# Kernel optimization log

Measured on AMD Instinct MI355X. Metric: run time of the kernel, lower is better.

Reference implementation:

```python
import jax, jax.numpy as jnp
import numpy as np

N, S, D, H, E, ETYPES = 1024, 64, 256, 4, 4096, 4
HD = D // H
EPS = 1e-5


def setup_inputs() -> dict:
    key = jax.random.key(0)
    ks = jax.random.split(key, 8)
    node_features = jax.random.normal(ks[0], (N, S, D), dtype=jnp.float32)
    lengths = jax.random.randint(ks[1], (N,), 1, S + 1)
    node_masks = (jnp.arange(S)[None, :] < lengths[:, None]).astype(jnp.float32)
    # unique edges (torch builds an adjacency matrix, so duplicates collapse)
    rng = np.random.default_rng(0)
    cand = rng.integers(0, N, size=(4 * E, 2))
    uniq = np.unique(cand, axis=0)
    assert uniq.shape[0] >= E
    perm = rng.permutation(uniq.shape[0])[:E]
    edge_index = jnp.asarray(uniq[perm].T, dtype=jnp.int64)  # [2, E]
    edge_type = jnp.asarray(rng.integers(1, ETYPES + 1, size=(E,)), dtype=jnp.int64)
    scale = 0.02
    wq = jax.random.normal(ks[2], (D, D), jnp.float32) * scale
    wk = jax.random.normal(ks[3], (D, D), jnp.float32) * scale
    wv = jax.random.normal(ks[4], (D, D), jnp.float32) * scale
    wo = jax.random.normal(ks[5], (D, D), jnp.float32) * scale
    return dict(
        node_features=node_features, node_masks=node_masks,
        ln_w=jnp.ones((D,), jnp.float32), ln_b=jnp.zeros((D,), jnp.float32),
        wq=wq, bq=jnp.zeros((D,), jnp.float32),
        wk=wk, bk=jnp.zeros((D,), jnp.float32),
        wv=wv, bv=jnp.zeros((D,), jnp.float32),
        wo=wo, bo=jnp.zeros((D,), jnp.float32),
        edge_type_weights=jnp.ones((ETYPES,), jnp.float32),
        edge_index=edge_index, edge_type=edge_type,
    )


def reference(node_features, node_masks, ln_w, ln_b, wq, bq, wk, bk, wv, bv,
              wo, bo, edge_type_weights, edge_index, edge_type):
    n, s, d = node_features.shape
    # LayerNorm (biased variance, eps=1e-5, as torch)
    mu = jnp.mean(node_features, axis=-1, keepdims=True)
    var = jnp.mean((node_features - mu) ** 2, axis=-1, keepdims=True)
    xn = (node_features - mu) * jax.lax.rsqrt(var + EPS) * ln_w + ln_b
    q = (xn @ wq + bq).reshape(n, s, H, HD)
    k = (xn @ wk + bk).reshape(n, s, H, HD)
    v = (xn @ wv + bv).reshape(n, s, H, HD)
    src, dst = edge_index[0], edge_index[1]
    # per-edge scalar bias: softplus(edge_type_weights[type-1]).clamp(1e-6, 1e6)
    ew = jnp.clip(jax.nn.softplus(edge_type_weights[edge_type - 1]), 1e-6, 1e6)  # [E]
    qe, ke, ve = q[src], k[dst], v[dst]              # [E,S,H,HD]
    km = node_masks[dst]                              # [E,S] key-side mask
    qm = node_masks[src]                              # [E,S] query-side mask
    scores = jnp.einsum('eqhd,ekhd->ehqk', qe, ke) / jnp.sqrt(jnp.float32(HD))
    scores = scores + ew[:, None, None, None]
    neg = jnp.float32(-1e30)
    scores = jnp.where(km[:, None, None, :] > 0, scores, neg)
    # per-edge softmax over the key node's valid tokens; zero rows where no valid key
    attn = jax.nn.softmax(scores, axis=-1) * km[:, None, None, :]
    ctx = jnp.einsum('ehqk,ekhd->eqhd', attn, ve) * qm[:, :, None, None]  # [E,S,H,HD]
    out = jax.ops.segment_sum(ctx, src, num_segments=n)   # sum over incident edges
    out = out.reshape(n, s, d)
    out = out @ wo + bo                                   # output projection (dropout=eval noop)
    out = out + node_features                             # residual
    return out * node_masks[..., None]
```

## Files before the change

kernel.cpp:

```cpp
#include <hip/hip_runtime.h>

#define DDIM 256
#define NEDGE 4096
#define SLEN 64
#define NNODE 1024
#define ROWS 65536

typedef short s16x8 __attribute__((ext_vector_type(8)));
typedef float f32x4 __attribute__((ext_vector_type(4)));

static __device__ __forceinline__ unsigned short f2bf(float f){
  union { float f; unsigned u; } v; v.f = f;
  unsigned r = v.u + 0x7FFFu + ((v.u >> 16) & 1u);
  return (unsigned short)(r >> 16);
}

static __device__ __forceinline__ void gl2lds16(const unsigned short* g, unsigned short* l){
  __builtin_amdgcn_global_load_lds((const __attribute__((address_space(1))) unsigned int*)g,
                                   (__attribute__((address_space(3))) unsigned int*)l, 16, 0, 0);
}

__global__ __launch_bounds__(256) void setup_kernel(const float* nf, const float* lnw, const float* lnb,
                                                    const float* wq, const float* wk, const float* wv, const float* wo,
                                                    const float* bq, const float* bk, const float* bv,
                                                    const float* masks, const int* eidx,
                                                    unsigned short* xn, unsigned short* Wqkv, unsigned short* Wo_t,
                                                    float* qkvb, int* lenp, int* startp, int* order, int* degp, int* elist){
  __shared__ int deg[NNODE];
  __shared__ int buf[256];
  __shared__ int hist[65];
  __shared__ int cur[NNODE];
  int bid = blockIdx.x, tid = threadIdx.x;
  if (bid < 16384){
    int lane = tid & 63;
    int row = bid*4 + (tid >> 6);
    const float4 x4 = ((const float4*)(nf + (size_t)row*DDIM))[lane];
    float s  = x4.x + x4.y + x4.z + x4.w;
    float sq = x4.x*x4.x + x4.y*x4.y + x4.z*x4.z + x4.w*x4.w;
    for (int off=1; off<64; off<<=1){ s += __shfl_xor(s, off); sq += __shfl_xor(sq, off); }
    float mu  = s  * (1.0f/DDIM);
    float var = sq * (1.0f/DDIM) - mu*mu;
    float rs  = rsqrtf(var + 1e-5f);
    float4 w4 = ((const float4*)lnw)[lane];
    float4 b4 = ((const float4*)lnb)[lane];
    ushort4 o;
    o.x = f2bf((x4.x - mu)*rs*w4.x + b4.x);
    o.y = f2bf((x4.y - mu)*rs*w4.y + b4.y);
    o.z = f2bf((x4.z - mu)*rs*w4.z + b4.z);
    o.w = f2bf((x4.w - mu)*rs*w4.w + b4.w);
    ((ushort4*)(xn + (size_t)row*DDIM))[lane] = o;
  } else if (bid < 17412){
    int idx = (bid - 16384)*256 + tid;
    if (idx < 196608){
      int mat = idx >> 16;
      int rem = idx & 65535;
      int n = rem >> 8, k = rem & 255;
      const float* W = (mat==0)?wq:(mat==1)?wk:wv;
      Wqkv[(size_t)(mat*256 + n)*256 + k] = f2bf(W[k*256 + n]);
    } else if (idx < 262144){
      int rem = idx - 196608;
      int n = rem >> 8, k = rem & 255;
      Wo_t[(size_t)n*256 + k] = f2bf(wo[k*256 + n]);
    } else if (idx < 262912){
      int i = idx - 262144;
      qkvb[i] = (i < 256) ? bq[i] : (i < 512) ? bk[i-256] : bv[i-512];
    }
  } else if (bid < 17668){
    int lane = tid & 63;
    int node = (bid - 17412)*4 + (tid >> 6);
    unsigned long long b = __ballot(masks[node*SLEN + lane] > 0.f);
    if (lane == 0) lenp[node] = __popcll(b);
  } else {
    int t = tid;
    #pragma unroll
    for (int i=0;i<4;i++) deg[i*256 + t] = 0;
    if (t < 65) hist[t] = 0;
    __syncthreads();
    #pragma unroll
    for (int i=0;i<16;i++) atomicAdd(&deg[eidx[i*256 + t]], 1);
    __syncthreads();
    int d[4]; int s = 0;
    #pragma unroll
    for (int j=0;j<4;j++){ d[j] = deg[t*4 + j]; s += d[j]; }
    buf[t] = s;
    __syncthreads();
    for (int off=1; off<256; off<<=1){
      int v = (t >= off) ? buf[t-off] : 0;
      __syncthreads();
      buf[t] += v;
      __syncthreads();
    }
    int run = buf[t] - s;
    #pragma unroll
    for (int j=0;j<4;j++){
      int node = t*4 + j;
      startp[node] = run; degp[node] = d[j]; cur[node] = run;
      run += d[j];
      int dc = d[j] > 64 ? 64 : d[j];
      atomicAdd(&hist[dc], 1);
    }
    __syncthreads();
    if (t == 0){
      int acc = 0;
      for (int i=64;i>=0;i--){ int h = hist[i]; hist[i] = acc; acc += h; }
    }
    __syncthreads();
    #pragma unroll
    for (int j=0;j<4;j++){
      int node = t*4 + j;
      int dc = d[j] > 64 ? 64 : d[j];
      int pos = atomicAdd(&hist[dc], 1);
      order[pos] = node;
    }
    __syncthreads();
    #pragma unroll
    for (int i=0;i<16;i++){
      int e = i*256 + t;
      int sn = eidx[e];
      int p = atomicAdd(&cur[sn], 1);
      elist[p] = eidx[NEDGE + e];
    }
  }
}

__global__ __launch_bounds__(256) void qkv_kernel(const unsigned short* xn, const unsigned short* Wqkv,
                                                  const float* qkvb, const int* lenp,
                                                  unsigned short* qb, unsigned short* kb_, unsigned short* vt){
  __shared__ __align__(16) unsigned short As[2][8192];
  __shared__ __align__(16) unsigned short Bs[2][8192];
  int tid = threadIdx.x;
  int lane = tid & 63, wid = tid >> 6, m = lane & 15, quad = lane >> 4;
  int row0 = blockIdx.x * 128;
  int nodeA = row0 >> 6;
  int vraA = ((lenp[nodeA]   + 15) >> 4) << 4;
  int vraB = ((lenp[nodeA+1] + 15) >> 4) << 4;
  int col0 = blockIdx.y * 128;
  int wr = wid & 1, wc = wid >> 1;
  int rbase = wr * 64;
  int nodeW = nodeA + wr;
  int qtmW = (wr ? vraB : vraA) >> 4;

  f32x4 acc[16];
  #pragma unroll
  for (int i=0;i<16;i++) acc[i] = (f32x4){0.f,0.f,0.f,0.f};

  #pragma unroll
  for (int i=0;i<4;i++){
    int rowg = i*32 + wid*8;
    bool ok = (rowg < 64) ? (rowg < vraA) : (rowg - 64 < vraB);
    if (ok){
      int cid = i*256 + tid, row = cid >> 3, c8 = cid & 7;
      gl2lds16(xn + (size_t)(row0 + row)*DDIM + ((c8 ^ (row&7))<<3), As[0] + cid*8);
    }
  }
  #pragma unroll
  for (int i=0;i<4;i++){
    int cid = i*256 + tid, row = cid >> 3, c8 = cid & 7;
    gl2lds16(Wqkv + (size_t)(col0 + row)*DDIM + ((c8 ^ (row&7))<<3), Bs[0] + cid*8);
  }

  for (int kc = 0; kc < 4; kc++){
    __syncthreads();
    if (kc < 3){
      int kn = kc + 1;
      #pragma unroll
      for (int i=0;i<4;i++){
        int rowg = i*32 + wid*8;
        bool ok = (rowg < 64) ? (rowg < vraA) : (rowg - 64 < vraB);
        if (ok){
          int cid = i*256 + tid, row = cid >> 3, c8 = cid & 7;
          gl2lds16(xn + (size_t)(row0 + row)*DDIM + kn*64 + ((c8 ^ (row&7))<<3), As[kn&1] + cid*8);
        }
      }
      #pragma unroll
      for (int i=0;i<4;i++){
        int cid = i*256 + tid, row = cid >> 3, c8 = cid & 7;
        gl2lds16(Wqkv + (size_t)(col0 + row)*DDIM + kn*64 + ((c8 ^ (row&7))<<3), Bs[kn&1] + cid*8);
      }
    }
    const unsigned short* Asc = As[kc&1];
    const unsigned short* Bsc = Bs[kc&1];
    #pragma unroll
    for (int ks=0; ks<2; ks++){
      int sw = ((ks*4 + quad) ^ (m&7)) << 3;
      s16x8 af[4], bf[4];
      #pragma unroll
      for (int mt=0;mt<4;mt++) if (mt < qtmW) af[mt] = *(const s16x8*)(Asc + (rbase + mt*16 + m)*64 + sw);
      #pragma unroll
      for (int nt=0;nt<4;nt++) bf[nt] = *(const s16x8*)(Bsc + (wc*64 + nt*16 + m)*64 + sw);
      #pragma unroll
      for (int mt=0;mt<4;mt++) if (mt < qtmW)
        #pragma unroll
        for (int nt=0;nt<4;nt++)
          acc[mt*4+nt] = __builtin_amdgcn_mfma_f32_16x16x32_bf16(af[mt], bf[nt], acc[mt*4+nt], 0,0,0);
    }
  }
  #pragma unroll
  for (int nt=0;nt<4;nt++){
    int cg = col0 + wc*64 + nt*16 + m;
    int mat = cg >> 8, col = cg & 255;
    float bb = qkvb[cg];
    if (mat < 2){
      unsigned short* ob = (mat==0)?qb:kb_;
      #pragma unroll
      for (int mt=0;mt<4;mt++) if (mt < qtmW)
        #pragma unroll
        for (int r=0;r<4;r++){
          int row = row0 + rbase + mt*16 + quad*4 + r;
          ob[(size_t)row*DDIM + col] = f2bf(acc[mt*4+nt][r] + bb);
        }
    } else {
      #pragma unroll
      for (int mt=0;mt<4;mt++) if (mt < qtmW){
        int tok0 = mt*16 + quad*4;
        ushort4 p;
        p.x = f2bf(acc[mt*4+nt][0] + bb);
        p.y = f2bf(acc[mt*4+nt][1] + bb);
        p.z = f2bf(acc[mt*4+nt][2] + bb);
        p.w = f2bf(acc[mt*4+nt][3] + bb);
        *(ushort4*)(vt + ((size_t)nodeW*256 + col)*64 + tok0) = p;
      }
    }
  }
}

__global__ __launch_bounds__(256) void attn_kernel(const unsigned short* qb, const unsigned short* kbuf,
                                                   const unsigned short* vtb, const int* lenp,
                                                   const int* startp, const int* degp, const int* elist,
                                                   const int* order, unsigned short* ctxb){
  __shared__ __align__(16) unsigned short Kt[2][4096];
  __shared__ __align__(16) unsigned short Vt[2][4096];
  __shared__ unsigned short P[4096];
  int tid = threadIdx.x;
  int lane = tid & 63, wid = tid >> 6, m = lane & 15, quad = lane >> 4;
  int src = order[blockIdx.x], h = blockIdx.y;
  int ls = lenp[src];
  int qtm = (ls + 15) >> 4;
  int s0 = startp[src], dg = degp[src];
  bool active = wid < qtm;
  unsigned short* Pw = P + wid*1024;

  s16x8 qf0 = {0,0,0,0,0,0,0,0}, qf1 = {0,0,0,0,0,0,0,0};
  if (active){
    const unsigned short* qbase = qb + (size_t)(src*SLEN + wid*16 + m)*DDIM + h*64 + quad*8;
    qf0 = *(const s16x8*)(qbase);
    qf1 = *(const s16x8*)(qbase + 32);
  }
  f32x4 o[4];
  #pragma unroll
  for (int i=0;i<4;i++) o[i] = (f32x4){0.f,0.f,0.f,0.f};

  int dst0 = 0, dst1 = 0, ld0 = 0;
  if (dg > 0){
    dst0 = elist[s0];
    ld0 = lenp[dst0];
    int kch = ((ld0 + 15) >> 4) * 128;
    #pragma unroll
    for (int i=0;i<2;i++){
      int cid = i*256 + tid;
      if (i*256 + wid*64 < kch){
        int row = cid >> 3, c8 = cid & 7;
        gl2lds16(kbuf + (size_t)(dst0*SLEN + row)*DDIM + h*64 + ((c8 ^ (row&7))<<3), Kt[0] + cid*8);
      }
    }
    const unsigned short* vhead = vtb + ((size_t)dst0*256 + h*64)*64;
    #pragma unroll
    for (int i=0;i<2;i++){
      int cid = i*256 + tid, row = cid >> 3, c8 = cid & 7;
      gl2lds16(vhead + row*64 + ((c8 ^ (row&7))<<3), Vt[0] + cid*8);
    }
  }
  if (dg > 1) dst1 = elist[s0 + 1];
  __syncthreads();

  for (int ei=0; ei<dg; ei++){
    int cur = ei & 1, nxt = cur ^ 1;
    int dst2 = (ei+2 < dg) ? elist[s0 + ei + 2] : 0;
    int ld1 = 0;
    if (ei+1 < dg){
      ld1 = lenp[dst1];
      int kch = ((ld1 + 15) >> 4) * 128;
      #pragma unroll
      for (int i=0;i<2;i++){
        int cid = i*256 + tid;
        if (i*256 + wid*64 < kch){
          int row = cid >> 3, c8 = cid & 7;
          gl2lds16(kbuf + (size_t)(dst1*SLEN + row)*DDIM + h*64 + ((c8 ^ (row&7))<<3), Kt[nxt] + cid*8);
        }
      }
      const unsigned short* vhead = vtb + ((size_t)dst1*256 + h*64)*64;
      #pragma unroll
      for (int i=0;i<2;i++){
        int cid = i*256 + tid, row = cid >> 3, c8 = cid & 7;
        gl2lds16(vhead + row*64 + ((c8 ^ (row&7))<<3), Vt[nxt] + cid*8);
      }
    }
    int ktm = (ld0 + 15) >> 4;
    int ks2 = (ktm + 1) >> 1;
    if (active){
      __builtin_amdgcn_s_setprio(1);
      f32x4 acc[4];
      #pragma unroll
      for (int i=0;i<4;i++) acc[i] = (f32x4){0.f,0.f,0.f,0.f};
      #pragma unroll
      for (int kt=0; kt<4; kt++) if (kt < ktm){
        int key = kt*16 + m;
        s16x8 b0 = *(const s16x8*)(Kt[cur] + key*64 + ((quad ^ (m&7))<<3));
        acc[kt] = __builtin_amdgcn_mfma_f32_16x16x32_bf16(qf0, b0, acc[kt], 0,0,0);
        s16x8 b1 = *(const s16x8*)(Kt[cur] + key*64 + (((4 + quad) ^ (m&7))<<3));
        acc[kt] = __builtin_amdgcn_mfma_f32_16x16x32_bf16(qf1, b1, acc[kt], 0,0,0);
      }
      #pragma unroll
      for (int r=0; r<4; r++){
        float x[4];
        #pragma unroll
        for (int kt=0; kt<4; kt++)
          x[kt] = (kt < ktm && kt*16 + m < ld0) ? __expf(acc[kt][r]*0.125f) : 0.f;
        float s = x[0] + x[1] + x[2] + x[3];
        for (int off=1; off<16; off<<=1) s += __shfl_xor(s, off);
        float inv = 1.0f / s;
        int q = quad*4 + r;
        #pragma unroll
        for (int kt=0; kt<4; kt++) if (kt < 2*ks2){
          int key = kt*16 + m;
          Pw[q*64 + (((key>>3)^(q&7))<<3) + (key&7)] = f2bf(x[kt]*inv);
        }
      }
      #pragma unroll
      for (int ks=0; ks<2; ks++) if (ks < ks2){
        s16x8 pa = *(const s16x8*)(Pw + m*64 + ((((ks*4+quad))^(m&7))<<3));
        #pragma unroll
        for (int dt=0; dt<4; dt++){
          int d = dt*16 + m;
          s16x8 vf = *(const s16x8*)(Vt[cur] + d*64 + (((ks*4+quad)^(d&7))<<3));
          o[dt] = __builtin_amdgcn_mfma_f32_16x16x32_bf16(pa, vf, o[dt], 0,0,0);
        }
      }
      __builtin_amdgcn_s_setprio(0);
    }
    dst0 = dst1; ld0 = ld1; dst1 = dst2;
    __syncthreads();
  }
  if (active){
    #pragma unroll
    for (int dt=0; dt<4; dt++){
      int col = h*64 + dt*16 + m;
      #pragma unroll
      for (int r=0; r<4; r++){
        int row = src*SLEN + wid*16 + quad*4 + r;
        ctxb[(size_t)row*DDIM + col] = f2bf(o[dt][r]);
      }
    }
  }
}

__global__ __launch_bounds__(256) void out_kernel(const unsigned short* ctxb, const unsigned short* Wo_t,
                                                  const float* bo, const float* nf, const float* masks,
                                                  const int* lenp, float* out){
  __shared__ __align__(16) unsigned short As[2][8192];
  __shared__ __align__(16) unsigned short Bs[2][8192];
  int tid = threadIdx.x;
  int lane = tid & 63, wid = tid >> 6, m = lane & 15, quad = lane >> 4;
  int row0 = blockIdx.x * 128;
  int nodeA = row0 >> 6;
  int vraA = ((lenp[nodeA]   + 15) >> 4) << 4;
  int vraB = ((lenp[nodeA+1] + 15) >> 4) << 4;
  int col0 = blockIdx.y * 128;
  int wr = wid & 1, wc = wid >> 1;
  int rbase = wr * 64;
  int qtmW = (wr ? vraB : vraA) >> 4;

  f32x4 acc[16];
  #pragma unroll
  for (int i=0;i<16;i++) acc[i] = (f32x4){0.f,0.f,0.f,0.f};

  #pragma unroll
  for (int i=0;i<4;i++){
    int rowg = i*32 + wid*8;
    bool ok = (rowg < 64) ? (rowg < vraA) : (rowg - 64 < vraB);
    if (ok){
      int cid = i*256 + tid, row = cid >> 3, c8 = cid & 7;
      gl2lds16(ctxb + (size_t)(row0 + row)*DDIM + ((c8 ^ (row&7))<<3), As[0] + cid*8);
    }
  }
  #pragma unroll
  for (int i=0;i<4;i++){
    int cid = i*256 + tid, row = cid >> 3, c8 = cid & 7;
    gl2lds16(Wo_t + (size_t)(col0 + row)*DDIM + ((c8 ^ (row&7))<<3), Bs[0] + cid*8);
  }

  for (int kc = 0; kc < 4; kc++){
    __syncthreads();
    if (kc < 3){
      int kn = kc + 1;
      #pragma unroll
      for (int i=0;i<4;i++){
        int rowg = i*32 + wid*8;
        bool ok = (rowg < 64) ? (rowg < vraA) : (rowg - 64 < vraB);
        if (ok){
          int cid = i*256 + tid, row = cid >> 3, c8 = cid & 7;
          gl2lds16(ctxb + (size_t)(row0 + row)*DDIM + kn*64 + ((c8 ^ (row&7))<<3), As[kn&1] + cid*8);
        }
      }
      #pragma unroll
      for (int i=0;i<4;i++){
        int cid = i*256 + tid, row = cid >> 3, c8 = cid & 7;
        gl2lds16(Wo_t + (size_t)(col0 + row)*DDIM + kn*64 + ((c8 ^ (row&7))<<3), Bs[kn&1] + cid*8);
      }
    }
    const unsigned short* Asc = As[kc&1];
    const unsigned short* Bsc = Bs[kc&1];
    #pragma unroll
    for (int ks=0; ks<2; ks++){
      int sw = ((ks*4 + quad) ^ (m&7)) << 3;
      s16x8 af[4], bf[4];
      #pragma unroll
      for (int mt=0;mt<4;mt++) if (mt < qtmW) af[mt] = *(const s16x8*)(Asc + (rbase + mt*16 + m)*64 + sw);
      #pragma unroll
      for (int nt=0;nt<4;nt++) bf[nt] = *(const s16x8*)(Bsc + (wc*64 + nt*16 + m)*64 + sw);
      #pragma unroll
      for (int mt=0;mt<4;mt++) if (mt < qtmW)
        #pragma unroll
        for (int nt=0;nt<4;nt++)
          acc[mt*4+nt] = __builtin_amdgcn_mfma_f32_16x16x32_bf16(af[mt], bf[nt], acc[mt*4+nt], 0,0,0);
    }
  }
  #pragma unroll
  for (int nt=0;nt<4;nt++){
    int col = col0 + wc*64 + nt*16 + m;
    float bb = bo[col];
    #pragma unroll
    for (int mt=0;mt<4;mt++){
      if (mt < qtmW){
        #pragma unroll
        for (int r=0;r<4;r++){
          int row = row0 + rbase + mt*16 + quad*4 + r;
          float v = acc[mt*4+nt][r] + bb + nf[(size_t)row*DDIM + col];
          out[(size_t)row*DDIM + col] = v * masks[row];
        }
      } else {
        #pragma unroll
        for (int r=0;r<4;r++){
          int row = row0 + rbase + mt*16 + quad*4 + r;
          out[(size_t)row*DDIM + col] = 0.f;
        }
      }
    }
  }
}

extern "C" void kernel_launch(void* const* d_in, const int* in_sizes, int n_in,
                              void* d_out, int out_size, void* d_ws, size_t ws_size,
                              hipStream_t stream){
  const float* nf    = (const float*)d_in[0];
  const float* masks = (const float*)d_in[1];
  const float* lnw   = (const float*)d_in[2];
  const float* lnb   = (const float*)d_in[3];
  const float* wq    = (const float*)d_in[4];
  const float* bq    = (const float*)d_in[5];
  const float* wk    = (const float*)d_in[6];
  const float* bk    = (const float*)d_in[7];
  const float* wv    = (const float*)d_in[8];
  const float* bv    = (const float*)d_in[9];
  const float* wo    = (const float*)d_in[10];
  const float* bo    = (const float*)d_in[11];
  const int*   eidx  = (const int*)d_in[13];
  float* out = (float*)d_out;

  char* ws = (char*)d_ws;
  const size_t B = (size_t)ROWS * DDIM * 2;
  unsigned short* xn   = (unsigned short*)(ws);
  unsigned short* qb   = (unsigned short*)(ws + B);
  unsigned short* kb   = (unsigned short*)(ws + 2*B);
  unsigned short* vt   = (unsigned short*)(ws + 3*B);
  unsigned short* ctxb = (unsigned short*)(ws + 4*B);
  char* wp = ws + 5*B;
  unsigned short* Wqkv = (unsigned short*)(wp);
  unsigned short* Wo_t = (unsigned short*)(wp + 393216);
  float* qkvb         = (float*)(wp + 524288);
  char* ip = wp + 528384;
  int* startp = (int*)(ip);
  int* lenp   = (int*)(ip + 4096);
  int* order  = (int*)(ip + 8192);
  int* degp   = (int*)(ip + 12288);
  int* elist  = (int*)(ip + 16384);

  setup_kernel<<<17669, 256, 0, stream>>>(nf, lnw, lnb, wq, wk, wv, wo, bq, bk, bv,
                                          masks, eidx, xn, Wqkv, Wo_t, qkvb,
                                          lenp, startp, order, degp, elist);
  qkv_kernel<<<dim3(ROWS/128, 6), 256, 0, stream>>>(xn, Wqkv, qkvb, lenp, qb, kb, vt);
  attn_kernel<<<dim3(NNODE, 4), 256, 0, stream>>>(qb, kb, vt, lenp, startp, degp, elist, order, ctxb);
  out_kernel<<<dim3(ROWS/128, 2), 256, 0, stream>>>(ctxb, Wo_t, bo, nf, masks, lenp, out);
}
```

Before: 343.9 us.

## Read K/V fragments straight from global memory instead of staged LDS double buffer

The attention kernel drops its cooperative, double-buffered async staging of each neighbour's K and V tiles into shared memory. Each wave now loads its MFMA operands directly from global (L2-resident) memory, and waves with no valid query tile exit early. Without shared K/V buffers the per-edge __syncthreads disappear, LDS use drops, and more blocks can be resident. In exchange, each active wave re-reads the same K/V data separately and there is no explicit prefetch overlapping the next edge's loads with compute.

```diff
diff --git a/kernel.cpp b/kernel.cpp
--- a/kernel.cpp
+++ b/kernel.cpp
@@ -228,128 +228,77 @@
                                                    const unsigned short* vtb, const int* lenp,
                                                    const int* startp, const int* degp, const int* elist,
                                                    const int* order, unsigned short* ctxb){
-  __shared__ __align__(16) unsigned short Kt[2][4096];
-  __shared__ __align__(16) unsigned short Vt[2][4096];
   __shared__ unsigned short P[4096];
   int tid = threadIdx.x;
   int lane = tid & 63, wid = tid >> 6, m = lane & 15, quad = lane >> 4;
   int src = order[blockIdx.x], h = blockIdx.y;
-  int ls = lenp[src];
-  int qtm = (ls + 15) >> 4;
+  int qtm = (lenp[src] + 15) >> 4;
+  if (wid >= qtm) return;
   int s0 = startp[src], dg = degp[src];
-  bool active = wid < qtm;
   unsigned short* Pw = P + wid*1024;
 
-  s16x8 qf0 = {0,0,0,0,0,0,0,0}, qf1 = {0,0,0,0,0,0,0,0};
-  if (active){
-    const unsigned short* qbase = qb + (size_t)(src*SLEN + wid*16 + m)*DDIM + h*64 + quad*8;
-    qf0 = *(const s16x8*)(qbase);
-    qf1 = *(const s16x8*)(qbase + 32);
-  }
+  const unsigned short* qbase = qb + (size_t)(src*SLEN + wid*16 + m)*DDIM + h*64 + quad*8;
+  s16x8 qf0 = *(const s16x8*)(qbase);
+  s16x8 qf1 = *(const s16x8*)(qbase + 32);
   f32x4 o[4];
   #pragma unroll
   for (int i=0;i<4;i++) o[i] = (f32x4){0.f,0.f,0.f,0.f};
 
-  int dst0 = 0, dst1 = 0, ld0 = 0;
-  if (dg > 0){
-    dst0 = elist[s0];
-    ld0 = lenp[dst0];
-    int kch = ((ld0 + 15) >> 4) * 128;
-    #pragma unroll
-    for (int i=0;i<2;i++){
-      int cid = i*256 + tid;
-      if (i*256 + wid*64 < kch){
-        int row = cid >> 3, c8 = cid & 7;
-        gl2lds16(kbuf + (size_t)(dst0*SLEN + row)*DDIM + h*64 + ((c8 ^ (row&7))<<3), Kt[0] + cid*8);
-      }
-    }
-    const unsigned short* vhead = vtb + ((size_t)dst0*256 + h*64)*64;
-    #pragma unroll
-    for (int i=0;i<2;i++){
-      int cid = i*256 + tid, row = cid >> 3, c8 = cid & 7;
-      gl2lds16(vhead + row*64 + ((c8 ^ (row&7))<<3), Vt[0] + cid*8);
-    }
-  }
-  if (dg > 1) dst1 = elist[s0 + 1];
-  __syncthreads();
-
+  int dstc = 0, ldc = 0;
+  if (dg > 0){ dstc = elist[s0]; ldc = lenp[dstc]; }
   for (int ei=0; ei<dg; ei++){
-    int cur = ei & 1, nxt = cur ^ 1;
-    int dst2 = (ei+2 < dg) ? elist[s0 + ei + 2] : 0;
-    int ld1 = 0;
-    if (ei+1 < dg){
-      ld1 = lenp[dst1];
-      int kch = ((ld1 + 15) >> 4) * 128;
-      #pragma unroll
-      for (int i=0;i<2;i++){
-        int cid = i*256 + tid;
-        if (i*256 + wid*64 < kch){
-          int row = cid >> 3, c8 = cid & 7;
-          gl2lds16(kbuf + (size_t)(dst1*SLEN + row)*DDIM + h*64 + ((c8 ^ (row&7))<<3), Kt[nxt] + cid*8);
-        }
-      }
-      const unsigned short* vhead = vtb + ((size_t)dst1*256 + h*64)*64;
-      #pragma unroll
-      for (int i=0;i<2;i++){
-        int cid = i*256 + tid, row = cid >> 3, c8 = cid & 7;
-        gl2lds16(vhead + row*64 + ((c8 ^ (row&7))<<3), Vt[nxt] + cid*8);
-      }
-    }
-    int ktm = (ld0 + 15) >> 4;
+    int dstn = 0, ldn = 0;
+    if (ei+1 < dg){ dstn = elist[s0+ei+1]; ldn = lenp[dstn]; }
+    int ktm = (ldc + 15) >> 4;
     int ks2 = (ktm + 1) >> 1;
-    if (active){
-      __builtin_amdgcn_s_setprio(1);
-      f32x4 acc[4];
-      #pragma unroll
-      for (int i=0;i<4;i++) acc[i] = (f32x4){0.f,0.f,0.f,0.f};
-      #pragma unroll
-      for (int kt=0; kt<4; kt++) if (kt < ktm){
+    const unsigned short* kb0 = kbuf + (size_t)dstc*SLEN*DDIM + h*64 + quad*8;
+    const unsigned short* vb0 = vtb + ((size_t)dstc*256 + h*64)*64;
+
+    f32x4 acc[4];
+    #pragma unroll
+    for (int i=0;i<4;i++) acc[i] = (f32x4){0.f,0.f,0.f,0.f};
+    #pragma unroll
+    for (int kt=0; kt<4; kt++) if (kt < ktm){
+      int key = kt*16 + m;
+      s16x8 b0 = *(const s16x8*)(kb0 + (size_t)key*DDIM);
+      s16x8 b1 = *(const s16x8*)(kb0 + (size_t)key*DDIM + 32);
+      acc[kt] = __builtin_amdgcn_mfma_f32_16x16x32_bf16(qf0, b0, acc[kt], 0,0,0);
+      acc[kt] = __builtin_amdgcn_mfma_f32_16x16x32_bf16(qf1, b1, acc[kt], 0,0,0);
+    }
+    #pragma unroll
+    for (int r=0; r<4; r++){
+      float x[4];
+      #pragma unroll
+      for (int kt=0; kt<4; kt++)
+        x[kt] = (kt < ktm && kt*16 + m < ldc) ? __expf(acc[kt][r]*0.125f) : 0.f;
+      float s = x[0] + x[1] + x[2] + x[3];
+      for (int off=1; off<16; off<<=1) s += __shfl_xor(s, off);
+      float inv = 1.0f / s;
+      int q = quad*4 + r;
+      #pragma unroll
+      for (int kt=0; kt<4; kt++) if (kt < 2*ks2){
         int key = kt*16 + m;
-        s16x8 b0 = *(const s16x8*)(Kt[cur] + key*64 + ((quad ^ (m&7))<<3));
-        acc[kt] = __builtin_amdgcn_mfma_f32_16x16x32_bf16(qf0, b0, acc[kt], 0,0,0);
-        s16x8 b1 = *(const s16x8*)(Kt[cur] + key*64 + (((4 + quad) ^ (m&7))<<3));
-        acc[kt] = __builtin_amdgcn_mfma_f32_16x16x32_bf16(qf1, b1, acc[kt], 0,0,0);
-      }
-      #pragma unroll
-      for (int r=0; r<4; r++){
-        float x[4];
-        #pragma unroll
-        for (int kt=0; kt<4; kt++)
-          x[kt] = (kt < ktm && kt*16 + m < ld0) ? __expf(acc[kt][r]*0.125f) : 0.f;
-        float s = x[0] + x[1] + x[2] + x[3];
-        for (int off=1; off<16; off<<=1) s += __shfl_xor(s, off);
-        float inv = 1.0f / s;
-        int q = quad*4 + r;
-        #pragma unroll
-        for (int kt=0; kt<4; kt++) if (kt < 2*ks2){
-          int key = kt*16 + m;
-          Pw[q*64 + (((key>>3)^(q&7))<<3) + (key&7)] = f2bf(x[kt]*inv);
-        }
-      }
-      #pragma unroll
-      for (int ks=0; ks<2; ks++) if (ks < ks2){
-        s16x8 pa = *(const s16x8*)(Pw + m*64 + ((((ks*4+quad))^(m&7))<<3));
-        #pragma unroll
-        for (int dt=0; dt<4; dt++){
-          int d = dt*16 + m;
-          s16x8 vf = *(const s16x8*)(Vt[cur] + d*64 + (((ks*4+quad)^(d&7))<<3));
-          o[dt] = __builtin_amdgcn_mfma_f32_16x16x32_bf16(pa, vf, o[dt], 0,0,0);
-        }
-      }
-      __builtin_amdgcn_s_setprio(0);
-    }
-    dst0 = dst1; ld0 = ld1; dst1 = dst2;
-    __syncthreads();
-  }
-  if (active){
-    #pragma unroll
-    for (int dt=0; dt<4; dt++){
-      int col = h*64 + dt*16 + m;
-      #pragma unroll
-      for (int r=0; r<4; r++){
-        int row = src*SLEN + wid*16 + quad*4 + r;
-        ctxb[(size_t)row*DDIM + col] = f2bf(o[dt][r]);
-      }
+        Pw[q*64 + (((key>>3)^(q&7))<<3) + (key&7)] = f2bf(x[kt]*inv);
+      }
+    }
+    #pragma unroll
+    for (int ks=0; ks<2; ks++) if (ks < ks2){
+      s16x8 pa = *(const s16x8*)(Pw + m*64 + (((ks*4+quad)^(m&7))<<3));
+      #pragma unroll
+      for (int dt=0; dt<4; dt++){
+        s16x8 vf = *(const s16x8*)(vb0 + (dt*16 + m)*64 + (ks*4+quad)*8);
+        o[dt] = __builtin_amdgcn_mfma_f32_16x16x32_bf16(pa, vf, o[dt], 0,0,0);
+      }
+    }
+    dstc = dstn; ldc = ldn;
+  }
+  #pragma unroll
+  for (int dt=0; dt<4; dt++){
+    int col = h*64 + dt*16 + m;
+    #pragma unroll
+    for (int r=0; r<4; r++){
+      int row = src*SLEN + wid*16 + quad*4 + r;
+      ctxb[(size_t)row*DDIM + col] = f2bf(o[dt][r]);
     }
   }
 }
```

Result: slower. 353.2 us (+2.7%).
